# Optimization experiments

Hardware: AMD Instinct MI355X
Metric: run time of the kernel (lower is better)

Reference implementation:

```python
import jax, jax.numpy as jnp
import numpy as np

# 26 neighbor taps of a 3x3x3 kernel in the exact order the torch module builds them:
# raster order over (z,y,x) in {0,1,2}^3, skipping the center (1,1,1).
OFFSETS = [(i, j, k) for i in range(3) for j in range(3) for k in range(3) if (i, j, k) != (1, 1, 1)]
DILATIONS = [1, 2]


def _affinity(x, d):
    # x: [B, K, D, H, W]; conv3d(kernel, dilation=d) on replicate-padded input is
    # exactly center-minus-shifted-neighbor with edge padding.
    B, K, D, H, W = x.shape
    xp = jnp.pad(x, ((0, 0), (0, 0), (d, d), (d, d), (d, d)), mode='edge')
    diffs = [x - xp[:, :, i * d:i * d + D, j * d:j * d + H * 0 + D if False else j * d + H, k * d:k * d + W]
             for (i, j, k) in OFFSETS]
    # fix slice bounds cleanly (depth D, height H, width W)
    diffs = [x - xp[:, :, i * d:i * d + D, j * d:j * d + H, k * d:k * d + W] for (i, j, k) in OFFSETS]
    return jnp.stack(diffs, axis=2)  # [B, K, 26, D, H, W]


def setup_inputs() -> dict:
    key = jax.random.key(0)
    x = jax.random.normal(key, (1, 2, 64, 128, 128), dtype=jnp.float32)
    return {"x": x}


def reference(x):
    # out: [B, K, 26*len(DILATIONS), D, H, W]
    affs = [_affinity(x, d) for d in DILATIONS]
    return jnp.concatenate(affs, axis=2)
```

## Files before the change

### kernel.cpp

```cpp
#include <hip/hip_runtime.h>


constexpr int Dz   = 64;
constexpr int Hy   = 128;
constexpr int Wx   = 128;
constexpr int HW   = Hy * Wx;
constexpr int DHW  = Dz * HW;
constexpr int TAPS = 52;

typedef float floatx4   __attribute__((ext_vector_type(4)));
typedef float floatx4_u __attribute__((ext_vector_type(4), aligned(4)));

__device__ __forceinline__ int iclamp(int v, int lo, int hi) {
    return v < lo ? lo : (v > hi ? hi : v);
}

__global__ __launch_bounds__(256)
void LocalAffinity_kernel(const float* __restrict__ in, float* __restrict__ out) {
    const int bid  = blockIdx.x;
    const int k    = bid & 1;
    const int rest = bid >> 1;
    const int t    = rest % TAPS;
    const int z    = rest / TAPS;

    const int d   = (t < 26) ? 1 : 2;
    const int t26 = (t < 26) ? t : t - 26;
    const int ras = (t26 < 13) ? t26 : t26 + 1;
    const int di  = ras / 9 - 1;
    const int dj  = (ras % 9) / 3 - 1;
    const int dk  = (ras % 3) - 1;
    const int dkd = dk * d;
    const int dy  = dj * d;
    const int zc  = iclamp(z + di * d, 0, Dz - 1);

    const float* __restrict__ ctr = in + k * DHW + z  * HW;
    const float* __restrict__ src = in + k * DHW + zc * HW;
    float* __restrict__ o = out + (size_t)(k * TAPS + t) * (size_t)DHW
                                + (size_t)z * HW;

    const int tid = threadIdx.x;

    #pragma unroll
    for (int i = 0; i < 16; ++i) {
        const int pos = (i << 8) | tid;
        const int y   = pos >> 5;
        const int x4  = pos & 31;
        const int x0  = x4 << 2;

        const floatx4 c = *(const floatx4*)(ctr + y * Wx + x0);

        const int yc = iclamp(y + dy, 0, Hy - 1);
        const float* row = src + yc * Wx;

        floatx4 s;
        if (dkd == 0) {
            s = *(const floatx4*)(row + x0);
        } else {
            const int xs  = x0 + dkd;
            const int xsa = iclamp(xs, 0, Wx - 4);
            const floatx4 v = *(const floatx4_u*)(row + xsa);
            s = v;
            if (dkd < 0) {
                const bool e = (x4 == 0);
                if (dkd == -1) {
                    if (e) { s.x = v.x; s.y = v.x; s.z = v.y; s.w = v.z; }
                } else {
                    if (e) { s.x = v.x; s.y = v.x; s.z = v.x; s.w = v.y; }
                }
            } else {
                const bool e = (x4 == 31);
                if (dkd == 1) {
                    if (e) { s.x = v.y; s.y = v.z; s.z = v.w; s.w = v.w; }
                } else {
                    if (e) { s.x = v.z; s.y = v.w; s.z = v.w; s.w = v.w; }
                }
            }
        }

        floatx4 r;
        r.x = c.x - s.x; r.y = c.y - s.y; r.z = c.z - s.z; r.w = c.w - s.w;
        *(floatx4*)(o + (size_t)pos * 4) = r;
    }
}

extern "C" void kernel_launch(void* const* d_in, const int* in_sizes, int n_in,
                              void* d_out, int out_size, void* d_ws, size_t ws_size,
                              hipStream_t stream) {
    const float* x = (const float*)d_in[0];
    float* out = (float*)d_out;
    LocalAffinity_kernel<<<2 * TAPS * Dz, 256, 0, stream>>>(x, out);
}
```

Before: 472.0 us.

## Compute all 52 taps per thread from register-cached rows and lane shuffles

```diff
diff --git a/kernel.cpp b/kernel.cpp
--- a/kernel.cpp
+++ b/kernel.cpp
@@ -8,8 +8,7 @@
 constexpr int DHW  = Dz * HW;
 constexpr int TAPS = 52;
 
-typedef float floatx4   __attribute__((ext_vector_type(4)));
-typedef float floatx4_u __attribute__((ext_vector_type(4), aligned(4)));
+typedef float floatx4 __attribute__((ext_vector_type(4)));
 
 __device__ __forceinline__ int iclamp(int v, int lo, int hi) {
     return v < lo ? lo : (v > hi ? hi : v);
@@ -17,69 +16,88 @@
 
 __global__ __launch_bounds__(256)
 void LocalAffinity_kernel(const float* __restrict__ in, float* __restrict__ out) {
-    const int bid  = blockIdx.x;
-    const int k    = bid & 1;
-    const int rest = bid >> 1;
-    const int t    = rest % TAPS;
-    const int z    = rest / TAPS;
+    const int b   = blockIdx.x;
+    const int k   = b & 1;
+    const int r2  = b >> 1;
+    const int z   = r2 & 63;
+    const int yg  = r2 >> 6;
+    const int tid = threadIdx.x;
+    const int y   = (yg << 3) | (tid >> 5);
+    const int x4  = tid & 31;
+    const int x0  = x4 << 2;
 
-    const int d   = (t < 26) ? 1 : 2;
-    const int t26 = (t < 26) ? t : t - 26;
-    const int ras = (t26 < 13) ? t26 : t26 + 1;
-    const int di  = ras / 9 - 1;
-    const int dj  = (ras % 9) / 3 - 1;
-    const int dk  = (ras % 3) - 1;
-    const int dkd = dk * d;
-    const int dy  = dj * d;
-    const int zc  = iclamp(z + di * d, 0, Dz - 1);
+    const float* __restrict__ base = in + k * DHW;
 
-    const float* __restrict__ ctr = in + k * DHW + z  * HW;
-    const float* __restrict__ src = in + k * DHW + zc * HW;
-    float* __restrict__ o = out + (size_t)(k * TAPS + t) * (size_t)DHW
-                                + (size_t)z * HW;
+    floatx4 r[2][3][3];
+    #pragma unroll
+    for (int dd = 0; dd < 2; ++dd) {
+        const int d = dd + 1;
+        #pragma unroll
+        for (int di = -1; di <= 1; ++di) {
+            #pragma unroll
+            for (int dj = -1; dj <= 1; ++dj) {
+                const int zc = iclamp(z + di * d, 0, Dz - 1);
+                const int yc = iclamp(y + dj * d, 0, Hy - 1);
+                r[dd][di + 1][dj + 1] =
+                    *(const floatx4*)(base + (zc * Hy + yc) * Wx + x0);
+            }
+        }
+    }
+    const floatx4 c = r[0][1][1];
 
-    const int tid = threadIdx.x;
+    float* __restrict__ obase = out + (size_t)k * ((size_t)TAPS * DHW)
+                                    + (size_t)((z * Hy + y) * Wx + x0);
 
     #pragma unroll
-    for (int i = 0; i < 16; ++i) {
-        const int pos = (i << 8) | tid;
-        const int y   = pos >> 5;
-        const int x4  = pos & 31;
-        const int x0  = x4 << 2;
+    for (int dd = 0; dd < 2; ++dd) {
+        #pragma unroll
+        for (int di = -1; di <= 1; ++di) {
+            #pragma unroll
+            for (int dj = -1; dj <= 1; ++dj) {
+                const floatx4 v = r[dd][di + 1][dj + 1];
+                #pragma unroll
+                for (int dk = -1; dk <= 1; ++dk) {
+                    if (di == 0 && dj == 0 && dk == 0) continue;
+                    const int raster = (di + 1) * 9 + (dj + 1) * 3 + (dk + 1);
+                    const int t26    = raster < 13 ? raster : raster - 1;
+                    const int t      = t26 + dd * 26;
 
-        const floatx4 c = *(const floatx4*)(ctr + y * Wx + x0);
+                    floatx4 s;
+                    if (dk == 0) {
+                        s = v;
+                    } else if (dk < 0) {
+                        if (dd == 0) {
+                            float sm = __shfl_up(v.w, 1);
+                            sm = (x4 == 0) ? v.x : sm;
+                            s.x = sm; s.y = v.x; s.z = v.y; s.w = v.z;
+                        } else {
+                            float a  = __shfl_up(v.z, 1);
+                            float bb = __shfl_up(v.w, 1);
+                            a  = (x4 == 0) ? v.x : a;
+                            bb = (x4 == 0) ? v.x : bb;
+                            s.x = a; s.y = bb; s.z = v.x; s.w = v.y;
+                        }
+                    } else {
+                        if (dd == 0) {
+                            float sp = __shfl_down(v.x, 1);
+                            sp = (x4 == 31) ? v.w : sp;
+                            s.x = v.y; s.y = v.z; s.z = v.w; s.w = sp;
+                        } else {
+                            float a  = __shfl_down(v.x, 1);
+                            float bb = __shfl_down(v.y, 1);
+                            a  = (x4 == 31) ? v.w : a;
+                            bb = (x4 == 31) ? v.w : bb;
+                            s.x = v.z; s.y = v.w; s.z = a; s.w = bb;
+                        }
+                    }
 
-        const int yc = iclamp(y + dy, 0, Hy - 1);
-        const float* row = src + yc * Wx;
-
-        floatx4 s;
-        if (dkd == 0) {
-            s = *(const floatx4*)(row + x0);
-        } else {
-            const int xs  = x0 + dkd;
-            const int xsa = iclamp(xs, 0, Wx - 4);
-            const floatx4 v = *(const floatx4_u*)(row + xsa);
-            s = v;
-            if (dkd < 0) {
-                const bool e = (x4 == 0);
-                if (dkd == -1) {
-                    if (e) { s.x = v.x; s.y = v.x; s.z = v.y; s.w = v.z; }
-                } else {
-                    if (e) { s.x = v.x; s.y = v.x; s.z = v.x; s.w = v.y; }
-                }
-            } else {
-                const bool e = (x4 == 31);
-                if (dkd == 1) {
-                    if (e) { s.x = v.y; s.y = v.z; s.z = v.w; s.w = v.w; }
-                } else {
-                    if (e) { s.x = v.z; s.y = v.w; s.z = v.w; s.w = v.w; }
+                    floatx4 o;
+                    o.x = c.x - s.x; o.y = c.y - s.y;
+                    o.z = c.z - s.z; o.w = c.w - s.w;
+                    *(floatx4*)(obase + (size_t)t * DHW) = o;
                 }
             }
         }
-
-        floatx4 r;
-        r.x = c.x - s.x; r.y = c.y - s.y; r.z = c.z - s.z; r.w = c.w - s.w;
-        *(floatx4*)(o + (size_t)pos * 4) = r;
     }
 }
 
@@ -88,5 +106,5 @@
                               hipStream_t stream) {
     const float* x = (const float*)d_in[0];
     float* out = (float*)d_out;
-    LocalAffinity_kernel<<<2 * TAPS * Dz, 256, 0, stream>>>(x, out);
+    LocalAffinity_kernel<<<2048, 256, 0, stream>>>(x, out);
 }
```

Measured after the change: 433.0 us. 8.3% less time.

## Split each plane into quarter blocks, remap block order, batch loads before stores

Applied to the files above, without the earlier changes.

```diff
diff --git a/kernel.cpp b/kernel.cpp
--- a/kernel.cpp
+++ b/kernel.cpp
@@ -17,11 +17,12 @@
 
 __global__ __launch_bounds__(256)
 void LocalAffinity_kernel(const float* __restrict__ in, float* __restrict__ out) {
-    const int bid  = blockIdx.x;
-    const int k    = bid & 1;
-    const int rest = bid >> 1;
-    const int t    = rest % TAPS;
-    const int z    = rest / TAPS;
+    const int bid = blockIdx.x;
+    const int q   = bid & 3;
+    const int z   = (bid >> 2) & 63;
+    const int b3  = bid >> 8;
+    const int t   = b3 % TAPS;
+    const int k   = b3 / TAPS;
 
     const int d   = (t < 26) ? 1 : 2;
     const int t26 = (t < 26) ? t : t - 26;
@@ -35,51 +36,57 @@
 
     const float* __restrict__ ctr = in + k * DHW + z  * HW;
     const float* __restrict__ src = in + k * DHW + zc * HW;
-    float* __restrict__ o = out + (size_t)(k * TAPS + t) * (size_t)DHW
-                                + (size_t)z * HW;
 
     const int tid = threadIdx.x;
+    const int x4  = tid & 31;
+    const int x0  = x4 << 2;
+    const int yb  = (q << 5) | (tid >> 5);
 
+    floatx4 c[4], s[4];
     #pragma unroll
-    for (int i = 0; i < 16; ++i) {
-        const int pos = (i << 8) | tid;
-        const int y   = pos >> 5;
-        const int x4  = pos & 31;
-        const int x0  = x4 << 2;
-
-        const floatx4 c = *(const floatx4*)(ctr + y * Wx + x0);
-
+    for (int p = 0; p < 4; ++p) {
+        const int y = yb + (p << 3);
+        c[p] = *(const floatx4*)(ctr + y * Wx + x0);
+    }
+    #pragma unroll
+    for (int p = 0; p < 4; ++p) {
+        const int y  = yb + (p << 3);
         const int yc = iclamp(y + dy, 0, Hy - 1);
         const float* row = src + yc * Wx;
-
-        floatx4 s;
         if (dkd == 0) {
-            s = *(const floatx4*)(row + x0);
+            s[p] = *(const floatx4*)(row + x0);
         } else {
-            const int xs  = x0 + dkd;
-            const int xsa = iclamp(xs, 0, Wx - 4);
+            const int xsa = iclamp(x0 + dkd, 0, Wx - 4);
             const floatx4 v = *(const floatx4_u*)(row + xsa);
-            s = v;
+            floatx4 sv = v;
             if (dkd < 0) {
                 const bool e = (x4 == 0);
                 if (dkd == -1) {
-                    if (e) { s.x = v.x; s.y = v.x; s.z = v.y; s.w = v.z; }
+                    if (e) { sv.x = v.x; sv.y = v.x; sv.z = v.y; sv.w = v.z; }
                 } else {
-                    if (e) { s.x = v.x; s.y = v.x; s.z = v.x; s.w = v.y; }
+                    if (e) { sv.x = v.x; sv.y = v.x; sv.z = v.x; sv.w = v.y; }
                 }
             } else {
                 const bool e = (x4 == 31);
                 if (dkd == 1) {
-                    if (e) { s.x = v.y; s.y = v.z; s.z = v.w; s.w = v.w; }
+                    if (e) { sv.x = v.y; sv.y = v.z; sv.z = v.w; sv.w = v.w; }
                 } else {
-                    if (e) { s.x = v.z; s.y = v.w; s.z = v.w; s.w = v.w; }
+                    if (e) { sv.x = v.z; sv.y = v.w; sv.z = v.w; sv.w = v.w; }
                 }
             }
+            s[p] = sv;
         }
+    }
 
+    float* __restrict__ obase = out + (size_t)(k * TAPS + t) * (size_t)DHW
+                                    + (size_t)z * HW;
+    #pragma unroll
+    for (int p = 0; p < 4; ++p) {
+        const int y = yb + (p << 3);
         floatx4 r;
-        r.x = c.x - s.x; r.y = c.y - s.y; r.z = c.z - s.z; r.w = c.w - s.w;
-        *(floatx4*)(o + (size_t)pos * 4) = r;
+        r.x = c[p].x - s[p].x; r.y = c[p].y - s[p].y;
+        r.z = c[p].z - s[p].z; r.w = c[p].w - s[p].w;
+        *(floatx4*)(obase + y * Wx + x0) = r;
     }
 }
 
@@ -88,5 +95,5 @@
                               hipStream_t stream) {
     const float* x = (const float*)d_in[0];
     float* out = (float*)d_out;
-    LocalAffinity_kernel<<<2 * TAPS * Dz, 256, 0, stream>>>(x, out);
+    LocalAffinity_kernel<<<2 * TAPS * Dz * 4, 256, 0, stream>>>(x, out);
 }
```

After: 427.1 us. 9.5% less time.
